# Kernel optimization log

Measured on AMD Instinct MI355X. Metric: run time of the kernel, lower is better.

The kernel has to match this reference:

```python
import jax, jax.numpy as jnp
import numpy as np

B, N, D, H = 2, 2048, 1024, 16
DH = D // H
MASK_VALUE = -1e7


def setup_inputs() -> dict:
    key = jax.random.key(0)
    ks = jax.random.split(key, 8)
    scale = 0.02
    return {
        "queries": jax.random.normal(ks[0], (B, N, D), dtype=jnp.float32),
        "keys": jax.random.normal(ks[1], (B, N, D), dtype=jnp.float32),
        "values": jax.random.normal(ks[2], (B, N, D), dtype=jnp.float32),
        "valid_len": jax.random.randint(ks[3], (B * H,), 1, N + 1, dtype=jnp.int32),
        "Wq": jax.random.normal(ks[4], (D, D), dtype=jnp.float32) * scale,
        "Wk": jax.random.normal(ks[5], (D, D), dtype=jnp.float32) * scale,
        "Wv": jax.random.normal(ks[6], (D, D), dtype=jnp.float32) * scale,
        "Wo": jax.random.normal(ks[7], (D, D), dtype=jnp.float32) * scale,
    }


def reference(queries, keys, values, valid_len, Wq, Wk, Wv, Wo):
    b, n, d = queries.shape
    h, dh = H, d // H

    def split_heads(x):  # (b, n, d) -> (b, h, n, dh)
        return x.reshape(b, n, h, dh).transpose(0, 2, 1, 3)

    q = split_heads(queries @ Wq)
    k = split_heads(keys @ Wk)
    v = split_heads(values @ Wv)

    # (b, h, nq, nk) full score tensor, as in the original naive bmm path
    scores = jnp.einsum("bhqd,bhkd->bhqk", q, k) / jnp.sqrt(jnp.float32(dh))

    # valid_len is 1-D of length b*h; repeat_interleave over queries means the
    # mask depends only on the key index: keep k < valid_len[bh]
    vl = valid_len.reshape(b, h, 1, 1)
    keep = jnp.arange(n)[None, None, None, :] < vl  # (b, h, 1, nk)
    scores = jnp.where(keep, scores, MASK_VALUE)

    attn = jax.nn.softmax(scores, axis=-1)
    heads = jnp.einsum("bhqk,bhkd->bhqd", attn, v)  # (b, h, n, dh)
    out = heads.transpose(0, 2, 1, 3).reshape(b, n, d) @ Wo
    return out
```

## Files before the change

kernel.cpp:

```cpp
#include <hip/hip_runtime.h>

#define B_ 2
#define N_ 2048
#define D_ 1024
#define H_ 16
#define DH_ 64
#define NITEMS 1024

typedef _Float16 half8 __attribute__((ext_vector_type(8)));
typedef _Float16 half4 __attribute__((ext_vector_type(4)));
typedef float f32x4 __attribute__((ext_vector_type(4)));

__device__ __forceinline__ void gl2lds16(const _Float16* g, _Float16* l) {
  __builtin_amdgcn_global_load_lds(
      (const __attribute__((address_space(1))) void*)g,
      (__attribute__((address_space(3))) void*)l, 16, 0, 0);
}

__global__ __launch_bounds__(256) void prep_kernel(
    const float* __restrict__ q, const float* __restrict__ k,
    const float* __restrict__ v, const float* __restrict__ Wq,
    const float* __restrict__ Wk, const float* __restrict__ Wv,
    const float* __restrict__ Wo, const int* __restrict__ vlen,
    _Float16* __restrict__ Xf, _Float16* __restrict__ WtAll,
    int* __restrict__ order) {
  __shared__ float tile[64][65];
  const int bid = blockIdx.x;
  if (bid < 6144) {
    int y = bid >> 11, x = bid & 2047;
    const float* s = (y == 0) ? q : (y == 1) ? k : v;
    _Float16* d = Xf + (size_t)y * ((size_t)B_ * N_ * D_);
    size_t idx = ((size_t)x * 256 + threadIdx.x) * 8;
    float4 a = *(const float4*)(s + idx);
    float4 b = *(const float4*)(s + idx + 4);
    half8 h;
    h[0] = (_Float16)a.x; h[1] = (_Float16)a.y; h[2] = (_Float16)a.z; h[3] = (_Float16)a.w;
    h[4] = (_Float16)b.x; h[5] = (_Float16)b.y; h[6] = (_Float16)b.z; h[7] = (_Float16)b.w;
    *(half8*)(d + idx) = h;
  } else if (bid < 6144 + 1024) {
    int idx = bid - 6144;
    int z = idx >> 8, rem = idx & 255, gy = rem >> 4, gx = rem & 15;
    const float* W = (z == 0) ? Wq : (z == 1) ? Wk : (z == 2) ? Wv : Wo;
    _Float16* Wt = WtAll + (size_t)z * D_ * D_;
    int k0 = gy * 64, n0 = gx * 64;
    int tr = threadIdx.x >> 4, tc = threadIdx.x & 15;
#pragma unroll
    for (int i = 0; i < 4; ++i) {
      int r = tr + i * 16;
      float4 va = *(const float4*)(W + (size_t)(k0 + r) * D_ + n0 + tc * 4);
      tile[r][tc * 4 + 0] = va.x; tile[r][tc * 4 + 1] = va.y;
      tile[r][tc * 4 + 2] = va.z; tile[r][tc * 4 + 3] = va.w;
    }
    __syncthreads();
#pragma unroll
    for (int i = 0; i < 4; ++i) {
      int r = tr + i * 16;
      half4 hv;
      hv[0] = (_Float16)tile[tc * 4 + 0][r];
      hv[1] = (_Float16)tile[tc * 4 + 1][r];
      hv[2] = (_Float16)tile[tc * 4 + 2][r];
      hv[3] = (_Float16)tile[tc * 4 + 3][r];
      *(half4*)(Wt + (size_t)(n0 + r) * D_ + k0 + tc * 4) = hv;
    }
  } else {
    int i = threadIdx.x;
    if (i < B_ * H_) {
      int vi = vlen[i], rank = 0;
      for (int j = 0; j < B_ * H_; ++j) {
        int vj = vlen[j];
        if (vj > vi || (vj == vi && j < i)) ++rank;
      }
      order[rank] = i;
    }
  }
}

#define BK 32

template <int NT, int MODE>
__global__ __launch_bounds__(256) void gemm_f16_kernel(
    const _Float16* __restrict__ Aall, const _Float16* __restrict__ Btall,
    _Float16* __restrict__ ChAll, float* __restrict__ Cf32) {
  constexpr int BN = NT * 32;
  constexpr int K = D_;
  __shared__ __attribute__((aligned(16))) _Float16 As[128 * BK];
  __shared__ __attribute__((aligned(16))) _Float16 Bs[BN * BK];
  const int z = blockIdx.z;
  const _Float16* A  = Aall  + (size_t)z * ((size_t)B_ * N_ * D_);
  const _Float16* Bt = Btall + (size_t)z * ((size_t)D_ * D_);
  _Float16* Chead = ChAll + (size_t)z * ((size_t)B_ * N_ * D_);

  const int tid = threadIdx.x;
  const int m0 = blockIdx.y * 128, n0 = blockIdx.x * BN;
  const int lane = tid & 63, w = tid >> 6;
  const int quad = lane >> 4, l15 = lane & 15;
  const int wm = (w >> 1) * 64, wn = (w & 1) * (BN / 2);
  const int swz = (quad ^ ((l15 >> 1) & 3)) * 8;
  f32x4 acc[4][NT] = {};

  for (int kt = 0; kt < K; kt += BK) {
    if (kt) __syncthreads();
#pragma unroll
    for (int p = 0; p < 2; ++p) {
      int c = p * 256 + tid;
      int row = c >> 2, pg = c & 3;
      int gl = pg ^ ((row >> 1) & 3);
      gl2lds16(A + (size_t)(m0 + row) * K + kt + gl * 8, &As[c * 8]);
    }
#pragma unroll
    for (int p = 0; p < NT / 2; ++p) {
      int c = p * 256 + tid;
      int row = c >> 2, pg = c & 3;
      int gl = pg ^ ((row >> 1) & 3);
      gl2lds16(Bt + (size_t)(n0 + row) * K + kt + gl * 8, &Bs[c * 8]);
    }
    __syncthreads();
    half8 af[4], bf[NT];
#pragma unroll
    for (int mt = 0; mt < 4; ++mt)
      af[mt] = *(const half8*)&As[(wm + mt * 16 + l15) * 32 + swz];
#pragma unroll
    for (int nt = 0; nt < NT; ++nt)
      bf[nt] = *(const half8*)&Bs[(wn + nt * 16 + l15) * 32 + swz];
#pragma unroll
    for (int mt = 0; mt < 4; ++mt)
#pragma unroll
      for (int nt = 0; nt < NT; ++nt)
        acc[mt][nt] = __builtin_amdgcn_mfma_f32_16x16x32_f16(
            af[mt], bf[nt], acc[mt][nt], 0, 0, 0);
  }

#pragma unroll
  for (int mt = 0; mt < 4; ++mt) {
    int mrow = m0 + wm + mt * 16 + quad * 4;
#pragma unroll
    for (int nt = 0; nt < NT; ++nt) {
      int jcol = n0 + wn + nt * 16 + l15;
#pragma unroll
      for (int r = 0; r < 4; ++r) {
        float val = acc[mt][nt][r];
        int m = mrow + r;
        if (MODE == 0) {
          int b = m >> 11, n = m & (N_ - 1);
          int h = jcol >> 6, dh = jcol & (DH_ - 1);
          Chead[((((size_t)(b * H_ + h)) * N_ + n) * DH_) + dh] = (_Float16)val;
        } else {
          Cf32[(size_t)m * D_ + jcol] = val;
        }
      }
    }
  }
}

__global__ __launch_bounds__(256) void transpose_v_kernel(
    const _Float16* __restrict__ Vh, _Float16* __restrict__ VtG) {
  __shared__ float Ls[64][65];
  int bh = blockIdx.y, k0 = blockIdx.x * 64;
  int tid = threadIdx.x;
  const _Float16* src = Vh + (size_t)bh * N_ * DH_;
#pragma unroll
  for (int p = 0; p < 2; ++p) {
    int c = p * 256 + tid, row = c >> 3, pg = c & 7;
    half8 hv = *(const half8*)(src + (size_t)(k0 + row) * DH_ + pg * 8);
#pragma unroll
    for (int u = 0; u < 8; ++u) Ls[row][pg * 8 + u] = (float)hv[u];
  }
  __syncthreads();
  _Float16* dst = VtG + (size_t)bh * N_ * DH_;
#pragma unroll
  for (int p = 0; p < 2; ++p) {
    int c = p * 256 + tid, dh = c >> 3, pg = c & 7;
    half8 hv;
#pragma unroll
    for (int u = 0; u < 8; ++u) hv[u] = (_Float16)Ls[pg * 8 + u][dh];
    *(half8*)(dst + (size_t)dh * N_ + k0 + pg * 8) = hv;
  }
}

__global__ __launch_bounds__(256, 4) void attn_kernel(
    const _Float16* __restrict__ Qh, const _Float16* __restrict__ Kh,
    const _Float16* __restrict__ VtG, const int* __restrict__ vlen,
    _Float16* __restrict__ Hd, const int* __restrict__ order) {
  __shared__ __attribute__((aligned(16))) _Float16 Ks[2][64 * 64];
  __shared__ __attribute__((aligned(16))) _Float16 Vt[2][64 * 64];
  const int tid = threadIdx.x, lane = tid & 63, w = tid >> 6;
  const int quad = lane >> 4, l15 = lane & 15;
  const int sw  = (quad ^ (l15 & 7)) * 8;
  const int sw2 = ((quad + 4) ^ (l15 & 7)) * 8;
  const float sc2 = 0.125f * 1.44269504088896f;
  const half4 ones = {(_Float16)1, (_Float16)1, (_Float16)1, (_Float16)1};

  const int item = blockIdx.x;
  const int bh = order[item >> 5];
  const int q0 = (item & 31) * 64;
  const int b = bh >> 4, h = bh & (H_ - 1);
  const int vl = vlen[bh];
  const int KT = (vl + 63) >> 6;
  const _Float16* Qb = Qh  + (size_t)bh * N_ * DH_;
  const _Float16* Kb = Kh  + (size_t)bh * N_ * DH_;
  const _Float16* Vb = VtG + (size_t)bh * N_ * DH_;

  const half8 qb0 = *(const half8*)(Qb + (size_t)(q0 + w * 16 + l15) * DH_ + quad * 8);
  const half8 qb1 = *(const half8*)(Qb + (size_t)(q0 + w * 16 + l15) * DH_ + 32 + quad * 8);

  half8 kpre[2], vpre[2];
  auto prefetch = [&](int k0k) {
#pragma unroll
    for (int p = 0; p < 2; ++p) {
      int c = p * 256 + tid;
      int row = c >> 3, pg = c & 7;
      kpre[p] = *(const half8*)(Kb + (size_t)(k0k + row) * DH_ + (pg ^ (row & 7)) * 8);
      vpre[p] = *(const half8*)(Vb + (size_t)row * N_ + k0k + pg * 8);
    }
  };
  auto commit = [&](int buf) {
#pragma unroll
    for (int p = 0; p < 2; ++p) {
      int c = p * 256 + tid;
      int row = c >> 3, pg = c & 7;
      *(half8*)&Ks[buf][c * 8] = kpre[p];
      int j0 = (pg * 2) ^ (row & 15), j1 = (pg * 2 + 1) ^ (row & 15);
      half4 lo = {vpre[p][0], vpre[p][1], vpre[p][2], vpre[p][3]};
      half4 hi = {vpre[p][4], vpre[p][5], vpre[p][6], vpre[p][7]};
      *(half4*)&Vt[buf][row * 64 + j0 * 4] = lo;
      *(half4*)&Vt[buf][row * 64 + j1 * 4] = hi;
    }
  };

  prefetch(0);
  commit(0);
  if (KT > 1) prefetch(64);
  __syncthreads();

  f32x4 Oacc[4] = {};
  f32x4 lacc = {};

  for (int kt = 0; kt < KT; ++kt) {
    const int cur = kt & 1;
    if (kt + 1 < KT) commit(1 - cur);
    if (kt + 2 < KT) prefetch((kt + 2) * 64);

    f32x4 s[4];
#pragma unroll
    for (int nt = 0; nt < 4; ++nt) {
      int r = nt * 16 + l15;
      half8 ka0 = *(const half8*)&Ks[cur][r * 64 + sw];
      half8 ka1 = *(const half8*)&Ks[cur][r * 64 + sw2];
      f32x4 c = {};
      c = __builtin_amdgcn_mfma_f32_16x16x32_f16(ka0, qb0, c, 0, 0, 0);
      c = __builtin_amdgcn_mfma_f32_16x16x32_f16(ka1, qb1, c, 0, 0, 0);
      s[nt] = c;
    }
    const int k0k = kt * 64;
    half4 pf[4];
    if (k0k + 64 <= vl) {
#pragma unroll
      for (int nt = 0; nt < 4; ++nt)
#pragma unroll
        for (int r = 0; r < 4; ++r)
          pf[nt][r] = (_Float16)exp2f(s[nt][r] * sc2);
    } else {
#pragma unroll
      for (int nt = 0; nt < 4; ++nt) {
        int keyb = k0k + nt * 16 + quad * 4;
#pragma unroll
        for (int r = 0; r < 4; ++r) {
          float p = exp2f(s[nt][r] * sc2);
          pf[nt][r] = (keyb + r < vl) ? (_Float16)p : (_Float16)0.f;
        }
      }
    }
#pragma unroll
    for (int nt = 0; nt < 4; ++nt) {
      lacc = __builtin_amdgcn_mfma_f32_16x16x16f16(ones, pf[nt], lacc, 0, 0, 0);
#pragma unroll
      for (int dt = 0; dt < 4; ++dt) {
        int dh = dt * 16 + l15;
        half4 va = *(const half4*)&Vt[cur][dh * 64 + (((nt * 4 + quad) ^ l15) << 2)];
        Oacc[dt] = __builtin_amdgcn_mfma_f32_16x16x16f16(va, pf[nt], Oacc[dt], 0, 0, 0);
      }
    }
    __syncthreads();
  }

  float inv_l = 1.0f / lacc[0];
  int q = q0 + w * 16 + l15;
  _Float16* out = Hd + ((size_t)(b * N_ + q)) * D_ + h * DH_;
#pragma unroll
  for (int dt = 0; dt < 4; ++dt) {
    half4 o;
#pragma unroll
    for (int r = 0; r < 4; ++r) o[r] = (_Float16)(Oacc[dt][r] * inv_l);
    *(half4*)(out + dt * 16 + quad * 4) = o;
  }
}

extern "C" void kernel_launch(void* const* d_in, const int* in_sizes, int n_in,
                              void* d_out, int out_size, void* d_ws, size_t ws_size,
                              hipStream_t stream) {
  const float* q  = (const float*)d_in[0];
  const float* k  = (const float*)d_in[1];
  const float* v  = (const float*)d_in[2];
  const int*   vl = (const int*)d_in[3];
  const float* Wq = (const float*)d_in[4];
  const float* Wk = (const float*)d_in[5];
  const float* Wv = (const float*)d_in[6];
  const float* Wo = (const float*)d_in[7];

  const size_t XSZ = (size_t)B_ * N_ * D_;
  const size_t WSZ = (size_t)D_ * D_;
  _Float16* ws = (_Float16*)d_ws;
  _Float16* Xf = ws;
  _Float16* Wt = Xf + 3 * XSZ;
  _Float16* Qh = Wt + 4 * WSZ;
  _Float16* Hd = Qh + 3 * XSZ;
  int* order = (int*)(Hd + XSZ);
  _Float16* VtG = Xf;

  prep_kernel<<<dim3(6144 + 1024 + 1), 256, 0, stream>>>(
      q, k, v, Wq, Wk, Wv, Wo, vl, Xf, Wt, order);

  gemm_f16_kernel<4, 0><<<dim3(D_ / 128, 32, 3), 256, 0, stream>>>(
      Xf, Wt, Qh, nullptr);

  transpose_v_kernel<<<dim3(N_ / 64, B_ * H_), 256, 0, stream>>>(
      Qh + 2 * XSZ, VtG);

  attn_kernel<<<dim3(NITEMS), 256, 0, stream>>>(
      Qh, Qh + XSZ, VtG, vl, Hd, order);

  gemm_f16_kernel<2, 1><<<dim3(D_ / 64, 32, 1), 256, 0, stream>>>(
      Hd, Wt + 3 * WSZ, nullptr, (float*)d_out);
}
```

Baseline: 222.6 us.

## Fuse V transpose into projection GEMM and make attention waves load K/V directly

The QKV projection GEMM now writes V directly in transposed per-head layout, which removes the separate transpose kernel and its extra pass over memory. The attention kernel drops LDS staging and block barriers. Each wave independently handles 32 queries and reads K and V fragments straight from global memory. Each wave now loads its own K/V, so global/L2 traffic per key tile goes up and the double-buffered prefetch overlap is lost. In exchange, occupancy and register use change because the launch bound hint was dropped.

```diff
diff --git a/kernel.cpp b/kernel.cpp
--- a/kernel.cpp
+++ b/kernel.cpp
@@ -5,7 +5,6 @@
 #define D_ 1024
 #define H_ 16
 #define DH_ 64
-#define NITEMS 1024
 
 typedef _Float16 half8 __attribute__((ext_vector_type(8)));
 typedef _Float16 half4 __attribute__((ext_vector_type(4)));
@@ -80,7 +79,8 @@
 template <int NT, int MODE>
 __global__ __launch_bounds__(256) void gemm_f16_kernel(
     const _Float16* __restrict__ Aall, const _Float16* __restrict__ Btall,
-    _Float16* __restrict__ ChAll, float* __restrict__ Cf32) {
+    _Float16* __restrict__ ChAll, _Float16* __restrict__ VtG,
+    float* __restrict__ Cf32) {
   constexpr int BN = NT * 32;
   constexpr int K = D_;
   __shared__ __attribute__((aligned(16))) _Float16 As[128 * BK];
@@ -136,162 +136,135 @@
 #pragma unroll
     for (int nt = 0; nt < NT; ++nt) {
       int jcol = n0 + wn + nt * 16 + l15;
-#pragma unroll
-      for (int r = 0; r < 4; ++r) {
-        float val = acc[mt][nt][r];
-        int m = mrow + r;
-        if (MODE == 0) {
-          int b = m >> 11, n = m & (N_ - 1);
-          int h = jcol >> 6, dh = jcol & (DH_ - 1);
-          Chead[((((size_t)(b * H_ + h)) * N_ + n) * DH_) + dh] = (_Float16)val;
-        } else {
-          Cf32[(size_t)m * D_ + jcol] = val;
+      if (MODE == 0 && z == 2) {
+        int b = mrow >> 11, key = mrow & (N_ - 1);
+        int h = jcol >> 6, dh = jcol & (DH_ - 1);
+        half4 o;
+#pragma unroll
+        for (int r = 0; r < 4; ++r) o[r] = (_Float16)acc[mt][nt][r];
+        *(half4*)(VtG + ((size_t)((b * H_ + h) * DH_ + dh)) * N_ + key) = o;
+      } else {
+#pragma unroll
+        for (int r = 0; r < 4; ++r) {
+          float val = acc[mt][nt][r];
+          int m = mrow + r;
+          if (MODE == 0) {
+            int b = m >> 11, n = m & (N_ - 1);
+            int h = jcol >> 6, dh = jcol & (DH_ - 1);
+            Chead[((((size_t)(b * H_ + h)) * N_ + n) * DH_) + dh] = (_Float16)val;
+          } else {
+            Cf32[(size_t)m * D_ + jcol] = val;
+          }
         }
       }
     }
   }
 }
 
-__global__ __launch_bounds__(256) void transpose_v_kernel(
-    const _Float16* __restrict__ Vh, _Float16* __restrict__ VtG) {
-  __shared__ float Ls[64][65];
-  int bh = blockIdx.y, k0 = blockIdx.x * 64;
-  int tid = threadIdx.x;
-  const _Float16* src = Vh + (size_t)bh * N_ * DH_;
-#pragma unroll
-  for (int p = 0; p < 2; ++p) {
-    int c = p * 256 + tid, row = c >> 3, pg = c & 7;
-    half8 hv = *(const half8*)(src + (size_t)(k0 + row) * DH_ + pg * 8);
-#pragma unroll
-    for (int u = 0; u < 8; ++u) Ls[row][pg * 8 + u] = (float)hv[u];
-  }
-  __syncthreads();
-  _Float16* dst = VtG + (size_t)bh * N_ * DH_;
-#pragma unroll
-  for (int p = 0; p < 2; ++p) {
-    int c = p * 256 + tid, dh = c >> 3, pg = c & 7;
-    half8 hv;
-#pragma unroll
-    for (int u = 0; u < 8; ++u) hv[u] = (_Float16)Ls[pg * 8 + u][dh];
-    *(half8*)(dst + (size_t)dh * N_ + k0 + pg * 8) = hv;
-  }
-}
-
-__global__ __launch_bounds__(256, 4) void attn_kernel(
+__global__ __launch_bounds__(256) void attn_kernel(
     const _Float16* __restrict__ Qh, const _Float16* __restrict__ Kh,
     const _Float16* __restrict__ VtG, const int* __restrict__ vlen,
     _Float16* __restrict__ Hd, const int* __restrict__ order) {
-  __shared__ __attribute__((aligned(16))) _Float16 Ks[2][64 * 64];
-  __shared__ __attribute__((aligned(16))) _Float16 Vt[2][64 * 64];
   const int tid = threadIdx.x, lane = tid & 63, w = tid >> 6;
   const int quad = lane >> 4, l15 = lane & 15;
-  const int sw  = (quad ^ (l15 & 7)) * 8;
-  const int sw2 = ((quad + 4) ^ (l15 & 7)) * 8;
-  const float sc2 = 0.125f * 1.44269504088896f;
-  const half4 ones = {(_Float16)1, (_Float16)1, (_Float16)1, (_Float16)1};
-
-  const int item = blockIdx.x;
-  const int bh = order[item >> 5];
-  const int q0 = (item & 31) * 64;
+  const int gid = blockIdx.x * 4 + w;
+  const int bh = order[gid >> 6];
+  const int q0 = (gid & 63) * 32;
   const int b = bh >> 4, h = bh & (H_ - 1);
   const int vl = vlen[bh];
   const int KT = (vl + 63) >> 6;
+  const float sc2 = 0.125f * 1.44269504088896f;
+  const half4 ones = {(_Float16)1, (_Float16)1, (_Float16)1, (_Float16)1};
+
   const _Float16* Qb = Qh  + (size_t)bh * N_ * DH_;
   const _Float16* Kb = Kh  + (size_t)bh * N_ * DH_;
   const _Float16* Vb = VtG + (size_t)bh * N_ * DH_;
 
-  const half8 qb0 = *(const half8*)(Qb + (size_t)(q0 + w * 16 + l15) * DH_ + quad * 8);
-  const half8 qb1 = *(const half8*)(Qb + (size_t)(q0 + w * 16 + l15) * DH_ + 32 + quad * 8);
-
-  half8 kpre[2], vpre[2];
-  auto prefetch = [&](int k0k) {
-#pragma unroll
-    for (int p = 0; p < 2; ++p) {
-      int c = p * 256 + tid;
-      int row = c >> 3, pg = c & 7;
-      kpre[p] = *(const half8*)(Kb + (size_t)(k0k + row) * DH_ + (pg ^ (row & 7)) * 8);
-      vpre[p] = *(const half8*)(Vb + (size_t)row * N_ + k0k + pg * 8);
-    }
-  };
-  auto commit = [&](int buf) {
-#pragma unroll
-    for (int p = 0; p < 2; ++p) {
-      int c = p * 256 + tid;
-      int row = c >> 3, pg = c & 7;
-      *(half8*)&Ks[buf][c * 8] = kpre[p];
-      int j0 = (pg * 2) ^ (row & 15), j1 = (pg * 2 + 1) ^ (row & 15);
-      half4 lo = {vpre[p][0], vpre[p][1], vpre[p][2], vpre[p][3]};
-      half4 hi = {vpre[p][4], vpre[p][5], vpre[p][6], vpre[p][7]};
-      *(half4*)&Vt[buf][row * 64 + j0 * 4] = lo;
-      *(half4*)&Vt[buf][row * 64 + j1 * 4] = hi;
-    }
-  };
-
-  prefetch(0);
-  commit(0);
-  if (KT > 1) prefetch(64);
-  __syncthreads();
-
-  f32x4 Oacc[4] = {};
-  f32x4 lacc = {};
+  half8 qb[2][2];
+#pragma unroll
+  for (int qh = 0; qh < 2; ++qh)
+#pragma unroll
+    for (int kk = 0; kk < 2; ++kk)
+      qb[qh][kk] = *(const half8*)(Qb + (size_t)(q0 + qh * 16 + l15) * DH_ +
+                                   kk * 32 + quad * 8);
+
+  f32x4 Oacc[4][2] = {};
+  f32x4 lacc[2] = {};
 
   for (int kt = 0; kt < KT; ++kt) {
-    const int cur = kt & 1;
-    if (kt + 1 < KT) commit(1 - cur);
-    if (kt + 2 < KT) prefetch((kt + 2) * 64);
-
-    f32x4 s[4];
-#pragma unroll
-    for (int nt = 0; nt < 4; ++nt) {
-      int r = nt * 16 + l15;
-      half8 ka0 = *(const half8*)&Ks[cur][r * 64 + sw];
-      half8 ka1 = *(const half8*)&Ks[cur][r * 64 + sw2];
-      f32x4 c = {};
-      c = __builtin_amdgcn_mfma_f32_16x16x32_f16(ka0, qb0, c, 0, 0, 0);
-      c = __builtin_amdgcn_mfma_f32_16x16x32_f16(ka1, qb1, c, 0, 0, 0);
-      s[nt] = c;
-    }
-    const int k0k = kt * 64;
-    half4 pf[4];
-    if (k0k + 64 <= vl) {
+    const int k0 = kt * 64;
+    half8 ka[4][2];
+#pragma unroll
+    for (int nt = 0; nt < 4; ++nt)
+#pragma unroll
+      for (int kk = 0; kk < 2; ++kk)
+        ka[nt][kk] = *(const half8*)(Kb + (size_t)(k0 + nt * 16 + l15) * DH_ +
+                                     kk * 32 + quad * 8);
+    half4 va[4][4];
+#pragma unroll
+    for (int dt = 0; dt < 4; ++dt)
 #pragma unroll
       for (int nt = 0; nt < 4; ++nt)
-#pragma unroll
-        for (int r = 0; r < 4; ++r)
-          pf[nt][r] = (_Float16)exp2f(s[nt][r] * sc2);
+        va[dt][nt] = *(const half4*)(Vb + (size_t)(dt * 16 + l15) * N_ + k0 +
+                                     (nt * 4 + quad) * 4);
+
+    f32x4 s[4][2];
+#pragma unroll
+    for (int nt = 0; nt < 4; ++nt)
+#pragma unroll
+      for (int qh = 0; qh < 2; ++qh) {
+        f32x4 c = {};
+        c = __builtin_amdgcn_mfma_f32_16x16x32_f16(ka[nt][0], qb[qh][0], c, 0, 0, 0);
+        c = __builtin_amdgcn_mfma_f32_16x16x32_f16(ka[nt][1], qb[qh][1], c, 0, 0, 0);
+        s[nt][qh] = c;
+      }
+    half4 pf[4][2];
+    if (k0 + 64 <= vl) {
+#pragma unroll
+      for (int nt = 0; nt < 4; ++nt)
+#pragma unroll
+        for (int qh = 0; qh < 2; ++qh)
+#pragma unroll
+          for (int r = 0; r < 4; ++r)
+            pf[nt][qh][r] = (_Float16)exp2f(s[nt][qh][r] * sc2);
     } else {
 #pragma unroll
       for (int nt = 0; nt < 4; ++nt) {
-        int keyb = k0k + nt * 16 + quad * 4;
-#pragma unroll
-        for (int r = 0; r < 4; ++r) {
-          float p = exp2f(s[nt][r] * sc2);
-          pf[nt][r] = (keyb + r < vl) ? (_Float16)p : (_Float16)0.f;
-        }
-      }
-    }
-#pragma unroll
-    for (int nt = 0; nt < 4; ++nt) {
-      lacc = __builtin_amdgcn_mfma_f32_16x16x16f16(ones, pf[nt], lacc, 0, 0, 0);
-#pragma unroll
-      for (int dt = 0; dt < 4; ++dt) {
-        int dh = dt * 16 + l15;
-        half4 va = *(const half4*)&Vt[cur][dh * 64 + (((nt * 4 + quad) ^ l15) << 2)];
-        Oacc[dt] = __builtin_amdgcn_mfma_f32_16x16x16f16(va, pf[nt], Oacc[dt], 0, 0, 0);
-      }
-    }
-    __syncthreads();
-  }
-
-  float inv_l = 1.0f / lacc[0];
-  int q = q0 + w * 16 + l15;
-  _Float16* out = Hd + ((size_t)(b * N_ + q)) * D_ + h * DH_;
-#pragma unroll
-  for (int dt = 0; dt < 4; ++dt) {
-    half4 o;
-#pragma unroll
-    for (int r = 0; r < 4; ++r) o[r] = (_Float16)(Oacc[dt][r] * inv_l);
-    *(half4*)(out + dt * 16 + quad * 4) = o;
+        int keyb = k0 + nt * 16 + quad * 4;
+#pragma unroll
+        for (int qh = 0; qh < 2; ++qh)
+#pragma unroll
+          for (int r = 0; r < 4; ++r) {
+            float p = exp2f(s[nt][qh][r] * sc2);
+            pf[nt][qh][r] = (keyb + r < vl) ? (_Float16)p : (_Float16)0.f;
+          }
+      }
+    }
+#pragma unroll
+    for (int nt = 0; nt < 4; ++nt)
+#pragma unroll
+      for (int qh = 0; qh < 2; ++qh) {
+        lacc[qh] = __builtin_amdgcn_mfma_f32_16x16x16f16(ones, pf[nt][qh],
+                                                         lacc[qh], 0, 0, 0);
+#pragma unroll
+        for (int dt = 0; dt < 4; ++dt)
+          Oacc[dt][qh] = __builtin_amdgcn_mfma_f32_16x16x16f16(
+              va[dt][nt], pf[nt][qh], Oacc[dt][qh], 0, 0, 0);
+      }
+  }
+
+#pragma unroll
+  for (int qh = 0; qh < 2; ++qh) {
+    float inv_l = 1.0f / lacc[qh][0];
+    int q = q0 + qh * 16 + l15;
+    _Float16* out = Hd + ((size_t)(b * N_ + q)) * D_ + h * DH_;
+#pragma unroll
+    for (int dt = 0; dt < 4; ++dt) {
+      half4 o;
+#pragma unroll
+      for (int r = 0; r < 4; ++r) o[r] = (_Float16)(Oacc[dt][qh][r] * inv_l);
+      *(half4*)(out + dt * 16 + quad * 4) = o;
+    }
   }
 }
 
@@ -310,25 +283,22 @@
   const size_t XSZ = (size_t)B_ * N_ * D_;
   const size_t WSZ = (size_t)D_ * D_;
   _Float16* ws = (_Float16*)d_ws;
-  _Float16* Xf = ws;
-  _Float16* Wt = Xf + 3 * XSZ;
-  _Float16* Qh = Wt + 4 * WSZ;
-  _Float16* Hd = Qh + 3 * XSZ;
+  _Float16* Xf  = ws;
+  _Float16* Wt  = Xf + 3 * XSZ;
+  _Float16* Qh  = Wt + 4 * WSZ;
+  _Float16* Kh  = Qh + XSZ;
+  _Float16* VtG = Kh + XSZ;
+  _Float16* Hd  = VtG + XSZ;
   int* order = (int*)(Hd + XSZ);
-  _Float16* VtG = Xf;
 
   prep_kernel<<<dim3(6144 + 1024 + 1), 256, 0, stream>>>(
       q, k, v, Wq, Wk, Wv, Wo, vl, Xf, Wt, order);
 
   gemm_f16_kernel<4, 0><<<dim3(D_ / 128, 32, 3), 256, 0, stream>>>(
-      Xf, Wt, Qh, nullptr);
-
-  transpose_v_kernel<<<dim3(N_ / 64, B_ * H_), 256, 0, stream>>>(
-      Qh + 2 * XSZ, VtG);
-
-  attn_kernel<<<dim3(NITEMS), 256, 0, stream>>>(
-      Qh, Qh + XSZ, VtG, vl, Hd, order);
+      Xf, Wt, Qh, VtG, nullptr);
+
+  attn_kernel<<<dim3(512), 256, 0, stream>>>(Qh, Kh, VtG, vl, Hd, order);
 
   gemm_f16_kernel<2, 1><<<dim3(D_ / 64, 32, 1), 256, 0, stream>>>(
-      Hd, Wt + 3 * WSZ, nullptr, (float*)d_out);
-}
+      Hd, Wt + 3 * WSZ, nullptr, nullptr, (float*)d_out);
+}
```

Result: slower. 297.4 us (+33.6%).
